# Performance work log

Hardware: AMD Instinct MI355X
Metric: run time of the kernel (lower is better)

## Reference

```python
import jax, jax.numpy as jnp
import numpy as np

P, G, N = 32, 256, 6890  # preds, gallery size, SMPL vertices per person


def _procrustes_v2v(pred, gt):
    """Similarity (Procrustes) align pred->gt, return mean per-vertex L2 error.
    pred, gt: (M, 3) point clouds (M = 2*N, both people jointly aligned)."""
    mu_p = pred.mean(axis=0)
    mu_g = gt.mean(axis=0)
    Xp = pred - mu_p
    Xg = gt - mu_g
    var_p = jnp.sum(Xp * Xp)
    K = Xp.T @ Xg                      # (3,3) cross-covariance
    U, s, Vh = jnp.linalg.svd(K)
    V = Vh.T
    d = jnp.sign(jnp.linalg.det(V @ U.T))  # reflection fix
    D = jnp.stack([jnp.ones_like(d), jnp.ones_like(d), d])
    R = (V * D[None, :]) @ U.T         # rotation, det(R)=+1
    scale = jnp.sum(s * D) / var_p
    aligned = scale * (Xp @ R.T) + mu_g
    return jnp.linalg.norm(aligned - gt, axis=-1).mean()


def setup_inputs() -> dict:
    key = jax.random.key(0)
    k1, k2 = jax.random.split(key)
    pred_vertices = jax.random.normal(k1, (P, 2, N, 3), dtype=jnp.float32)
    target = jax.random.normal(k2, (G, 2, N, 3), dtype=jnp.float32)
    return {"pred_vertices": pred_vertices, "target": target}


def reference(pred_vertices, target):
    # flatten the two-person meshes into a single joint point cloud per sample
    pred = pred_vertices.reshape(pred_vertices.shape[0], -1, 3)  # (P, 2N, 3)
    gt = target.reshape(target.shape[0], -1, 3)                  # (G, 2N, 3)
    # all-pairs procrustes v2v errors: (P, G)
    pair_err = jax.vmap(lambda p: jax.vmap(lambda g: _procrustes_v2v(p, g))(gt))(pred)
    mapping = jnp.argmin(pair_err, axis=1)   # best gt index per prediction
    min_error = jnp.min(pair_err, axis=1)    # its v2v error
    return mapping, min_error
```

## Files before the change

### kernel.cpp

```cpp
#include <hip/hip_runtime.h>
#include <math.h>

#define P_ 32
#define G_ 256
#define NV 6890
#define M_ (2 * NV)
#define QUADS (M_ / 4)
#define NPAIR (P_ * G_)
#define NB_CC 512

typedef float v2f __attribute__((ext_vector_type(2)));
__device__ inline v2f v2(float a, float b) { v2f r; r.x = a; r.y = b; return r; }
__device__ inline v2f vsplat(float a) { v2f r; r.x = a; r.y = a; return r; }
__device__ inline v2f vfma(v2f a, v2f b, v2f c) { return __builtin_elementwise_fma(a, b, c); }

struct WS {
    float mu_p[P_][3];
    float var_p[P_];
    float mu_g[G_][3];
    float At[NPAIR][12];
    float Kmat[NPAIR][9];
    float pair_err[NPAIR];
};

__device__ inline double block_reduce(double v, double* smem) {
#pragma unroll
    for (int off = 32; off > 0; off >>= 1) v += __shfl_down(v, off, 64);
    int wid  = threadIdx.x >> 6;
    int lane = threadIdx.x & 63;
    __syncthreads();
    if (lane == 0) smem[wid] = v;
    __syncthreads();
    double r = 0.0;
    if (threadIdx.x == 0) {
        int nw = blockDim.x >> 6;
        for (int w = 0; w < nw; ++w) r += smem[w];
    }
    return r;
}

__global__ __launch_bounds__(256, 2) void crosscov_p(const float* __restrict__ pred,
                                                     const float* __restrict__ gt,
                                                     WS* __restrict__ ws) {
    int bx = blockIdx.x;
    int t = threadIdx.x;

    if (bx >= NB_CC) {
        int b = bx - NB_CC;
        bool isP = (b < P_);
        const float* base = isP ? pred + (size_t)b * (M_ * 3)
                                : gt + (size_t)(b - P_) * (M_ * 3);
        double sx = 0, sy = 0, sz = 0, sq = 0;
        for (int q = t; q < QUADS; q += 256) {
            const float4* p4 = (const float4*)(base + 12 * (size_t)q);
            float4 a = p4[0], c = p4[1], d = p4[2];
            sx += (double)a.x + (double)a.w + (double)c.z + (double)d.y;
            sy += (double)a.y + (double)c.x + (double)c.w + (double)d.z;
            sz += (double)a.z + (double)c.y + (double)d.x + (double)d.w;
            if (isP) {
                sq += (double)a.x * a.x + (double)a.y * a.y + (double)a.z * a.z +
                      (double)a.w * a.w + (double)c.x * c.x + (double)c.y * c.y +
                      (double)c.z * c.z + (double)c.w * c.w + (double)d.x * d.x +
                      (double)d.y * d.y + (double)d.z * d.z + (double)d.w * d.w;
            }
        }
        __shared__ double smem[4];
        double rx = block_reduce(sx, smem);
        double ry = block_reduce(sy, smem);
        double rz = block_reduce(sz, smem);
        double rq = block_reduce(sq, smem);
        if (t == 0) {
            double mx = rx / M_, my = ry / M_, mz = rz / M_;
            if (isP) {
                ws->mu_p[b][0] = (float)mx;
                ws->mu_p[b][1] = (float)my;
                ws->mu_p[b][2] = (float)mz;
                ws->var_p[b] = (float)(rq - (mx * mx + my * my + mz * mz) * (double)M_);
            } else {
                ws->mu_g[b - P_][0] = (float)mx;
                ws->mu_g[b - P_][1] = (float)my;
                ws->mu_g[b - P_][2] = (float)mz;
            }
        }
        return;
    }

    int gbase = (bx & 63) * 4;
    int pbase = (bx >> 6) * 4;
    const float* pb[4];
    const float* gb[4];
#pragma unroll
    for (int j = 0; j < 4; ++j) {
        pb[j] = pred + (size_t)(pbase + j) * (M_ * 3);
        gb[j] = gt + (size_t)(gbase + j) * (M_ * 3);
    }

    v2f a01[16], a34[16], a67[16], a25[16];
    float a8[16];
#pragma unroll
    for (int i = 0; i < 16; ++i) {
        a01[i] = vsplat(0.f); a34[i] = vsplat(0.f);
        a67[i] = vsplat(0.f); a25[i] = vsplat(0.f);
        a8[i] = 0.f;
    }

    for (int q = t; q < QUADS; q += 256) {
        float4 P[4][3];
#pragma unroll
        for (int j = 0; j < 4; ++j) {
            const float4* p4 = (const float4*)(pb[j] + 12 * (size_t)q);
            P[j][0] = p4[0]; P[j][1] = p4[1]; P[j][2] = p4[2];
        }
#pragma unroll
        for (int gg = 0; gg < 4; ++gg) {
            const float4* g4 = (const float4*)(gb[gg] + 12 * (size_t)q);
            float4 Ga = g4[0], Gc = g4[1], Gd = g4[2];
            v2f gxy0 = v2(Ga.x, Ga.y), gxy1 = v2(Ga.w, Gc.x);
            v2f gxy2 = v2(Gc.z, Gc.w), gxy3 = v2(Gd.y, Gd.z);
            float gz0 = Ga.z, gz1 = Gc.y, gz2 = Gd.x, gz3 = Gd.w;
#pragma unroll
            for (int pp = 0; pp < 4; ++pp) {
                int i = gg * 4 + pp;
                float4 Pa = P[pp][0], Pc = P[pp][1], Pd = P[pp][2];
                a01[i] = vfma(vsplat(Pa.x), gxy0, a01[i]);
                a34[i] = vfma(vsplat(Pa.y), gxy0, a34[i]);
                a67[i] = vfma(vsplat(Pa.z), gxy0, a67[i]);
                a25[i] = vfma(v2(Pa.x, Pa.y), vsplat(gz0), a25[i]);
                a8[i]  = fmaf(Pa.z, gz0, a8[i]);
                a01[i] = vfma(vsplat(Pa.w), gxy1, a01[i]);
                a34[i] = vfma(vsplat(Pc.x), gxy1, a34[i]);
                a67[i] = vfma(vsplat(Pc.y), gxy1, a67[i]);
                a25[i] = vfma(v2(Pa.w, Pc.x), vsplat(gz1), a25[i]);
                a8[i]  = fmaf(Pc.y, gz1, a8[i]);
                a01[i] = vfma(vsplat(Pc.z), gxy2, a01[i]);
                a34[i] = vfma(vsplat(Pc.w), gxy2, a34[i]);
                a67[i] = vfma(vsplat(Pd.x), gxy2, a67[i]);
                a25[i] = vfma(v2(Pc.z, Pc.w), vsplat(gz2), a25[i]);
                a8[i]  = fmaf(Pd.x, gz2, a8[i]);
                a01[i] = vfma(vsplat(Pd.y), gxy3, a01[i]);
                a34[i] = vfma(vsplat(Pd.z), gxy3, a34[i]);
                a67[i] = vfma(vsplat(Pd.w), gxy3, a67[i]);
                a25[i] = vfma(v2(Pd.y, Pd.z), vsplat(gz3), a25[i]);
                a8[i]  = fmaf(Pd.w, gz3, a8[i]);
            }
        }
    }

    float K[16][9];
#pragma unroll
    for (int i = 0; i < 16; ++i) {
        K[i][0] = a01[i].x; K[i][1] = a01[i].y; K[i][2] = a25[i].x;
        K[i][3] = a34[i].x; K[i][4] = a34[i].y; K[i][5] = a25[i].y;
        K[i][6] = a67[i].x; K[i][7] = a67[i].y; K[i][8] = a8[i];
    }

#pragma unroll
    for (int i = 0; i < 16; ++i)
#pragma unroll
        for (int j = 0; j < 9; ++j) {
            float v = K[i][j];
            v += __shfl_xor(v, 1);  v += __shfl_xor(v, 2);
            v += __shfl_xor(v, 4);  v += __shfl_xor(v, 8);
            v += __shfl_xor(v, 16); v += __shfl_xor(v, 32);
            K[i][j] = v;
        }
    __shared__ float part[4][144];
    int lane = t & 63, wave = t >> 6;
    if (lane == 0) {
#pragma unroll
        for (int i = 0; i < 16; ++i)
#pragma unroll
            for (int j = 0; j < 9; ++j) part[wave][i * 9 + j] = K[i][j];
    }
    __syncthreads();
    if (t < 144) {
        float s = part[0][t] + part[1][t] + part[2][t] + part[3][t];
        int idx = t / 9, j = t % 9;
        int gg = idx >> 2, pp = idx & 3;
        ws->Kmat[(gbase + gg) * P_ + (pbase + pp)][j] = s;
    }
}

__global__ __launch_bounds__(256) void pair_svd(WS* ws) {
    int pair = blockIdx.x * blockDim.x + threadIdx.x;
    if (pair >= NPAIR) return;
    int p = pair & 31;
    int g = pair >> 5;

    double K[3][3];
#pragma unroll
    for (int a = 0; a < 3; ++a)
#pragma unroll
        for (int b = 0; b < 3; ++b) K[a][b] = (double)ws->Kmat[pair][3 * a + b];
    {
        double mp[3] = { ws->mu_p[p][0], ws->mu_p[p][1], ws->mu_p[p][2] };
        double mg[3] = { ws->mu_g[g][0], ws->mu_g[g][1], ws->mu_g[g][2] };
#pragma unroll
        for (int a = 0; a < 3; ++a)
#pragma unroll
            for (int b = 0; b < 3; ++b)
                K[a][b] -= (double)M_ * mp[a] * mg[b];
    }

    double S[3][3];
#pragma unroll
    for (int a = 0; a < 3; ++a)
#pragma unroll
        for (int b = 0; b < 3; ++b) {
            double acc = 0.0;
#pragma unroll
            for (int c = 0; c < 3; ++c) acc += K[c][a] * K[c][b];
            S[a][b] = acc;
        }

    double V[3][3] = { {1, 0, 0}, {0, 1, 0}, {0, 0, 1} };
    double tr = S[0][0] + S[1][1] + S[2][2];
    double tol = 1e-30 * tr * tr + 1e-300;
    const int PP[3] = {0, 0, 1};
    const int QQ[3] = {1, 2, 2};
    for (int sweep = 0; sweep < 30; ++sweep) {
        double off = S[0][1] * S[0][1] + S[0][2] * S[0][2] + S[1][2] * S[1][2];
        if (off <= tol) break;
        for (int r3 = 0; r3 < 3; ++r3) {
            int pq = PP[r3], qq = QQ[r3];
            double apq = S[pq][qq];
            if (apq == 0.0) continue;
            double theta = (S[qq][qq] - S[pq][pq]) / (2.0 * apq);
            double tt = copysign(1.0, theta) / (fabs(theta) + sqrt(theta * theta + 1.0));
            double c = 1.0 / sqrt(tt * tt + 1.0);
            double sj = tt * c;
            for (int r = 0; r < 3; ++r) {
                double srp = S[r][pq], srq = S[r][qq];
                S[r][pq] = c * srp - sj * srq;
                S[r][qq] = sj * srp + c * srq;
            }
            for (int cc = 0; cc < 3; ++cc) {
                double spr = S[pq][cc], sqr = S[qq][cc];
                S[pq][cc] = c * spr - sj * sqr;
                S[qq][cc] = sj * spr + c * sqr;
            }
            for (int r = 0; r < 3; ++r) {
                double vrp = V[r][pq], vrq = V[r][qq];
                V[r][pq] = c * vrp - sj * vrq;
                V[r][qq] = sj * vrp + c * vrq;
            }
        }
    }

    double lam[3] = { S[0][0], S[1][1], S[2][2] };
    int idx[3] = { 0, 1, 2 };
    if (lam[idx[0]] < lam[idx[1]]) { int tt = idx[0]; idx[0] = idx[1]; idx[1] = tt; }
    if (lam[idx[0]] < lam[idx[2]]) { int tt = idx[0]; idx[0] = idx[2]; idx[2] = tt; }
    if (lam[idx[1]] < lam[idx[2]]) { int tt = idx[1]; idx[1] = idx[2]; idx[2] = tt; }
    double Vs[3][3];
    double sv[3];
#pragma unroll
    for (int i = 0; i < 3; ++i) {
        double l = lam[idx[i]];
        sv[i] = sqrt(l > 0.0 ? l : 0.0);
        for (int r = 0; r < 3; ++r) Vs[r][i] = V[r][idx[i]];
    }

    double U[3][3];
#pragma unroll
    for (int i = 0; i < 3; ++i) {
        double kx = K[0][0] * Vs[0][i] + K[0][1] * Vs[1][i] + K[0][2] * Vs[2][i];
        double ky = K[1][0] * Vs[0][i] + K[1][1] * Vs[1][i] + K[1][2] * Vs[2][i];
        double kz = K[2][0] * Vs[0][i] + K[2][1] * Vs[1][i] + K[2][2] * Vs[2][i];
        double inv = (sv[i] > 1e-12 * sv[0] && sv[i] > 0.0) ? 1.0 / sv[i] : 0.0;
        U[0][i] = kx * inv; U[1][i] = ky * inv; U[2][i] = kz * inv;
    }
    if (sv[2] <= 1e-12 * sv[0] || sv[0] == 0.0) {
        U[0][2] = U[1][0] * U[2][1] - U[2][0] * U[1][1];
        U[1][2] = U[2][0] * U[0][1] - U[0][0] * U[2][1];
        U[2][2] = U[0][0] * U[1][1] - U[1][0] * U[0][1];
    }

    double detK = K[0][0] * (K[1][1] * K[2][2] - K[1][2] * K[2][1])
                - K[0][1] * (K[1][0] * K[2][2] - K[1][2] * K[2][0])
                + K[0][2] * (K[1][0] * K[2][1] - K[1][1] * K[2][0]);
    double d = (detK >= 0.0) ? 1.0 : -1.0;

    double varp = (double)ws->var_p[p];
    double scale = (sv[0] + sv[1] + d * sv[2]) / varp;

    float A[9];
#pragma unroll
    for (int a = 0; a < 3; ++a)
#pragma unroll
        for (int b = 0; b < 3; ++b) {
            double r = Vs[a][0] * U[b][0] + Vs[a][1] * U[b][1] + d * Vs[a][2] * U[b][2];
            A[3 * a + b] = (float)(scale * r);
        }
    double mp[3] = { ws->mu_p[p][0], ws->mu_p[p][1], ws->mu_p[p][2] };
    double mg[3] = { ws->mu_g[g][0], ws->mu_g[g][1], ws->mu_g[g][2] };
    float tvec[3];
#pragma unroll
    for (int a = 0; a < 3; ++a)
        tvec[a] = (float)(mg[a] - ((double)A[3 * a + 0] * mp[0] + (double)A[3 * a + 1] * mp[1] +
                                   (double)A[3 * a + 2] * mp[2]));

#pragma unroll
    for (int j = 0; j < 9; ++j) ws->At[pair][j] = A[j];
#pragma unroll
    for (int j = 0; j < 3; ++j) ws->At[pair][9 + j] = tvec[j];
}

__global__ __launch_bounds__(256, 3) void pair_error_p(const float* __restrict__ pred,
                                                       const float* __restrict__ gt,
                                                       WS* __restrict__ ws) {
    int bx = blockIdx.x;
    int gbase = (bx & 63) * 4;
    int pbase = (bx >> 6) * 2;
    int t = threadIdx.x;

    v2f a03[8], a14[8], a25v[8], t01[8];
    float a6[8], a7[8], a8v[8], t2[8];
#pragma unroll
    for (int gg = 0; gg < 4; ++gg)
#pragma unroll
        for (int pp = 0; pp < 2; ++pp) {
            int i = gg * 2 + pp;
            const float* At = ws->At[(gbase + gg) * P_ + (pbase + pp)];
            a03[i] = v2(At[0], At[3]);
            a14[i] = v2(At[1], At[4]);
            a25v[i] = v2(At[2], At[5]);
            t01[i] = v2(At[9], At[10]);
            a6[i] = At[6]; a7[i] = At[7]; a8v[i] = At[8]; t2[i] = At[11];
        }

    const float* pb0 = pred + (size_t)pbase * (M_ * 3);
    const float* pb1 = pred + (size_t)(pbase + 1) * (M_ * 3);
    const float* gb[4];
#pragma unroll
    for (int j = 0; j < 4; ++j) gb[j] = gt + (size_t)(gbase + j) * (M_ * 3);

    float acc[8];
#pragma unroll
    for (int i = 0; i < 8; ++i) acc[i] = 0.f;

    for (int q = t; q < QUADS; q += 256) {
        float4 P[2][3];
        {
            const float4* p4 = (const float4*)(pb0 + 12 * (size_t)q);
            P[0][0] = p4[0]; P[0][1] = p4[1]; P[0][2] = p4[2];
            p4 = (const float4*)(pb1 + 12 * (size_t)q);
            P[1][0] = p4[0]; P[1][1] = p4[1]; P[1][2] = p4[2];
        }
#pragma unroll
        for (int gg = 0; gg < 4; ++gg) {
            const float4* g4 = (const float4*)(gb[gg] + 12 * (size_t)q);
            float4 Ga = g4[0], Gc = g4[1], Gd = g4[2];
            v2f gxy[4] = { v2(Ga.x, Ga.y), v2(Ga.w, Gc.x), v2(Gc.z, Gc.w), v2(Gd.y, Gd.z) };
            float gz[4] = { Ga.z, Gc.y, Gd.x, Gd.w };
#pragma unroll
            for (int pp = 0; pp < 2; ++pp) {
                int i = gg * 2 + pp;
                float4 Pa = P[pp][0], Pc = P[pp][1], Pd = P[pp][2];
                float x[4] = { Pa.x, Pa.w, Pc.z, Pd.y };
                float y[4] = { Pa.y, Pc.x, Pc.w, Pd.z };
                float z[4] = { Pa.z, Pc.y, Pd.x, Pd.w };
                float s = 0.f;
#pragma unroll
                for (int k = 0; k < 4; ++k) {
                    v2f dd = vfma(a03[i], vsplat(x[k]),
                             vfma(a14[i], vsplat(y[k]),
                             vfma(a25v[i], vsplat(z[k]), t01[i])));
                    dd = dd - gxy[k];
                    float dz = fmaf(a6[i], x[k], fmaf(a7[i], y[k], fmaf(a8v[i], z[k], t2[i]))) - gz[k];
                    v2f m = dd * dd;
                    s += __builtin_amdgcn_sqrtf(fmaf(dz, dz, m.x + m.y));
                }
                acc[i] += s;
            }
        }
    }

#pragma unroll
    for (int i = 0; i < 8; ++i) {
        float v = acc[i];
        v += __shfl_xor(v, 1);  v += __shfl_xor(v, 2);
        v += __shfl_xor(v, 4);  v += __shfl_xor(v, 8);
        v += __shfl_xor(v, 16); v += __shfl_xor(v, 32);
        acc[i] = v;
    }
    __shared__ float part[4][8];
    int lane = t & 63, wave = t >> 6;
    if (lane == 0) {
#pragma unroll
        for (int i = 0; i < 8; ++i) part[wave][i] = acc[i];
    }
    __syncthreads();
    if (t < 8) {
        float s = part[0][t] + part[1][t] + part[2][t] + part[3][t];
        int gg = t >> 1, pp = t & 1;
        ws->pair_err[(gbase + gg) * P_ + (pbase + pp)] = s / (float)M_;
    }
}

__global__ void argmin_out(const WS* __restrict__ ws, float* __restrict__ out) {
    __shared__ float be[8][32];
    __shared__ int   bg[8][32];
    int t = threadIdx.x;
    int p = t & 31, slice = t >> 5;
    float best = 3.4e38f;
    int bi = G_;
    for (int g = slice; g < G_; g += 8) {
        float e = ws->pair_err[g * P_ + p];
        if (e < best) { best = e; bi = g; }
    }
    be[slice][p] = best;
    bg[slice][p] = bi;
    __syncthreads();
    if (t < P_) {
        float b0 = be[0][t];
        int   i0 = bg[0][t];
        for (int s = 1; s < 8; ++s) {
            float e = be[s][t];
            int   i = bg[s][t];
            if (e < b0 || (e == b0 && i < i0)) { b0 = e; i0 = i; }
        }
        out[t] = (float)i0;
        out[P_ + t] = b0;
    }
}

extern "C" void kernel_launch(void* const* d_in, const int* in_sizes, int n_in,
                              void* d_out, int out_size, void* d_ws, size_t ws_size,
                              hipStream_t stream) {
    const float* pred = (const float*)d_in[0];
    const float* gt   = (const float*)d_in[1];
    float* out = (float*)d_out;
    WS* ws = (WS*)d_ws;

    crosscov_p<<<dim3(NB_CC + P_ + G_), dim3(256), 0, stream>>>(pred, gt, ws);
    pair_svd<<<dim3(NPAIR / 256), dim3(256), 0, stream>>>(ws);
    pair_error_p<<<dim3(16 * 64), dim3(256), 0, stream>>>(pred, gt, ws);
    argmin_out<<<dim3(1), dim3(256), 0, stream>>>(ws, out);
}
```

Measured before the change: 211.8 us.

## Repack point clouds into SoA workspace with fused stats, use in crosscov and error

Adds a repack kernel that transposes each sample's interleaved xyz into a structure-of-arrays copy in the workspace through LDS, and accumulates means and variance with double atomics. The cross-covariance and error kernels then read contiguous X/Y/Z float4 streams instead of strided AoS triples, which removes shuffling of lanes and lets stats run as a separate, better-parallelised pass. pair_svd now uses 64-thread blocks and reads stats directly. The price is an extra full read and write of the inputs (about 30 MB), a memset and an atomic reduction. The old path is kept as a fallback when the workspace is too small.

```diff
diff --git a/kernel.cpp b/kernel.cpp
--- a/kernel.cpp
+++ b/kernel.cpp
@@ -8,6 +8,9 @@
 #define QUADS (M_ / 4)
 #define NPAIR (P_ * G_)
 #define NB_CC 512
+#define SAMPLES (P_ + G_)
+#define NCHUNK 14
+#define SAMPLE_F4 (3 * QUADS)
 
 typedef float v2f __attribute__((ext_vector_type(2)));
 __device__ inline v2f v2(float a, float b) { v2f r; r.x = a; r.y = b; return r; }
@@ -15,6 +18,8 @@
 __device__ inline v2f vfma(v2f a, v2f b, v2f c) { return __builtin_elementwise_fma(a, b, c); }
 
 struct WS {
+    double stat[SAMPLES][4];
+    float soa[SAMPLES * 3 * M_];
     float mu_p[P_][3];
     float var_p[P_];
     float mu_g[G_][3];
@@ -39,60 +44,77 @@
     return r;
 }
 
-__global__ __launch_bounds__(256, 2) void crosscov_p(const float* __restrict__ pred,
-                                                     const float* __restrict__ gt,
-                                                     WS* __restrict__ ws) {
+__global__ __launch_bounds__(256) void repack_stats(const float* __restrict__ pred,
+                                                    const float* __restrict__ gt,
+                                                    WS* __restrict__ ws) {
     int bx = blockIdx.x;
+    int s = bx / NCHUNK;
+    int chunk = bx - s * NCHUNK;
+    bool isP = (s < P_);
+    const float4* src4 = (const float4*)(isP ? pred + (size_t)s * (M_ * 3)
+                                             : gt + (size_t)(s - P_) * (M_ * 3));
+    __shared__ __align__(16) float lds[256 * 12];
     int t = threadIdx.x;
-
-    if (bx >= NB_CC) {
-        int b = bx - NB_CC;
-        bool isP = (b < P_);
-        const float* base = isP ? pred + (size_t)b * (M_ * 3)
-                                : gt + (size_t)(b - P_) * (M_ * 3);
-        double sx = 0, sy = 0, sz = 0, sq = 0;
-        for (int q = t; q < QUADS; q += 256) {
-            const float4* p4 = (const float4*)(base + 12 * (size_t)q);
-            float4 a = p4[0], c = p4[1], d = p4[2];
-            sx += (double)a.x + (double)a.w + (double)c.z + (double)d.y;
-            sy += (double)a.y + (double)c.x + (double)c.w + (double)d.z;
-            sz += (double)a.z + (double)c.y + (double)d.x + (double)d.w;
-            if (isP) {
-                sq += (double)a.x * a.x + (double)a.y * a.y + (double)a.z * a.z +
-                      (double)a.w * a.w + (double)c.x * c.x + (double)c.y * c.y +
-                      (double)c.z * c.z + (double)c.w * c.w + (double)d.x * d.x +
-                      (double)d.y * d.y + (double)d.z * d.z + (double)d.w * d.w;
-            }
-        }
-        __shared__ double smem[4];
-        double rx = block_reduce(sx, smem);
-        double ry = block_reduce(sy, smem);
-        double rz = block_reduce(sz, smem);
-        double rq = block_reduce(sq, smem);
-        if (t == 0) {
-            double mx = rx / M_, my = ry / M_, mz = rz / M_;
-            if (isP) {
-                ws->mu_p[b][0] = (float)mx;
-                ws->mu_p[b][1] = (float)my;
-                ws->mu_p[b][2] = (float)mz;
-                ws->var_p[b] = (float)(rq - (mx * mx + my * my + mz * mz) * (double)M_);
-            } else {
-                ws->mu_g[b - P_][0] = (float)mx;
-                ws->mu_g[b - P_][1] = (float)my;
-                ws->mu_g[b - P_][2] = (float)mz;
-            }
-        }
-        return;
-    }
-
+    int f4base = chunk * (256 * 3);
+#pragma unroll
+    for (int k = 0; k < 3; ++k) {
+        int f4 = f4base + k * 256 + t;
+        if (f4 < SAMPLE_F4) ((float4*)lds)[k * 256 + t] = src4[f4];
+    }
+    __syncthreads();
+    int q = chunk * 256 + t;
+    double sx = 0, sy = 0, sz = 0, sq = 0;
+    if (q < QUADS) {
+        const float* v = lds + 12 * t;
+        float4 X = make_float4(v[0], v[3], v[6], v[9]);
+        float4 Y = make_float4(v[1], v[4], v[7], v[10]);
+        float4 Z = make_float4(v[2], v[5], v[8], v[11]);
+        float4* dst = (float4*)ws->soa;
+        dst[(size_t)(s * 3 + 0) * QUADS + q] = X;
+        dst[(size_t)(s * 3 + 1) * QUADS + q] = Y;
+        dst[(size_t)(s * 3 + 2) * QUADS + q] = Z;
+        sx = (double)X.x + (double)X.y + (double)X.z + (double)X.w;
+        sy = (double)Y.x + (double)Y.y + (double)Y.z + (double)Y.w;
+        sz = (double)Z.x + (double)Z.y + (double)Z.z + (double)Z.w;
+        if (isP) {
+            sq = (double)X.x * X.x + (double)X.y * X.y + (double)X.z * X.z +
+                 (double)X.w * X.w + (double)Y.x * Y.x + (double)Y.y * Y.y +
+                 (double)Y.z * Y.z + (double)Y.w * Y.w + (double)Z.x * Z.x +
+                 (double)Z.y * Z.y + (double)Z.z * Z.z + (double)Z.w * Z.w;
+        }
+    }
+    __shared__ double smem[4];
+    double rx = block_reduce(sx, smem);
+    double ry = block_reduce(sy, smem);
+    double rz = block_reduce(sz, smem);
+    double rq = block_reduce(sq, smem);
+    if (t == 0) {
+        atomicAdd(&ws->stat[s][0], rx);
+        atomicAdd(&ws->stat[s][1], ry);
+        atomicAdd(&ws->stat[s][2], rz);
+        if (isP) atomicAdd(&ws->stat[s][3], rq);
+    }
+}
+
+#define CC_VERT(i, px, py, pz, gxy, gz)                  \
+    a01[i] = vfma(vsplat(px), gxy, a01[i]);              \
+    a34[i] = vfma(vsplat(py), gxy, a34[i]);              \
+    a67[i] = vfma(vsplat(pz), gxy, a67[i]);              \
+    a25[i] = vfma(v2(px, py), vsplat(gz), a25[i]);       \
+    a8[i]  = fmaf(pz, gz, a8[i]);
+
+__global__ __launch_bounds__(256, 2) void crosscov_soa(WS* __restrict__ ws) {
+    int bx = blockIdx.x;
     int gbase = (bx & 63) * 4;
     int pbase = (bx >> 6) * 4;
-    const float* pb[4];
-    const float* gb[4];
+    int t = threadIdx.x;
+    const float4* soa4 = (const float4*)ws->soa;
+    const float4* pb[4];
+    const float4* gb[4];
 #pragma unroll
     for (int j = 0; j < 4; ++j) {
-        pb[j] = pred + (size_t)(pbase + j) * (M_ * 3);
-        gb[j] = gt + (size_t)(gbase + j) * (M_ * 3);
+        pb[j] = soa4 + (size_t)(pbase + j) * SAMPLE_F4;
+        gb[j] = soa4 + (size_t)(P_ + gbase + j) * SAMPLE_F4;
     }
 
     v2f a01[16], a34[16], a67[16], a25[16];
@@ -105,43 +127,27 @@
     }
 
     for (int q = t; q < QUADS; q += 256) {
-        float4 P[4][3];
+        float4 PX[4], PY[4], PZ[4];
 #pragma unroll
         for (int j = 0; j < 4; ++j) {
-            const float4* p4 = (const float4*)(pb[j] + 12 * (size_t)q);
-            P[j][0] = p4[0]; P[j][1] = p4[1]; P[j][2] = p4[2];
+            PX[j] = pb[j][q];
+            PY[j] = pb[j][QUADS + q];
+            PZ[j] = pb[j][2 * QUADS + q];
         }
 #pragma unroll
         for (int gg = 0; gg < 4; ++gg) {
-            const float4* g4 = (const float4*)(gb[gg] + 12 * (size_t)q);
-            float4 Ga = g4[0], Gc = g4[1], Gd = g4[2];
-            v2f gxy0 = v2(Ga.x, Ga.y), gxy1 = v2(Ga.w, Gc.x);
-            v2f gxy2 = v2(Gc.z, Gc.w), gxy3 = v2(Gd.y, Gd.z);
-            float gz0 = Ga.z, gz1 = Gc.y, gz2 = Gd.x, gz3 = Gd.w;
+            float4 GX = gb[gg][q];
+            float4 GY = gb[gg][QUADS + q];
+            float4 GZ = gb[gg][2 * QUADS + q];
+            v2f gxy0 = v2(GX.x, GY.x), gxy1 = v2(GX.y, GY.y);
+            v2f gxy2 = v2(GX.z, GY.z), gxy3 = v2(GX.w, GY.w);
 #pragma unroll
             for (int pp = 0; pp < 4; ++pp) {
                 int i = gg * 4 + pp;
-                float4 Pa = P[pp][0], Pc = P[pp][1], Pd = P[pp][2];
-                a01[i] = vfma(vsplat(Pa.x), gxy0, a01[i]);
-                a34[i] = vfma(vsplat(Pa.y), gxy0, a34[i]);
-                a67[i] = vfma(vsplat(Pa.z), gxy0, a67[i]);
-                a25[i] = vfma(v2(Pa.x, Pa.y), vsplat(gz0), a25[i]);
-                a8[i]  = fmaf(Pa.z, gz0, a8[i]);
-                a01[i] = vfma(vsplat(Pa.w), gxy1, a01[i]);
-                a34[i] = vfma(vsplat(Pc.x), gxy1, a34[i]);
-                a67[i] = vfma(vsplat(Pc.y), gxy1, a67[i]);
-                a25[i] = vfma(v2(Pa.w, Pc.x), vsplat(gz1), a25[i]);
-                a8[i]  = fmaf(Pc.y, gz1, a8[i]);
-                a01[i] = vfma(vsplat(Pc.z), gxy2, a01[i]);
-                a34[i] = vfma(vsplat(Pc.w), gxy2, a34[i]);
-                a67[i] = vfma(vsplat(Pd.x), gxy2, a67[i]);
-                a25[i] = vfma(v2(Pc.z, Pc.w), vsplat(gz2), a25[i]);
-                a8[i]  = fmaf(Pd.x, gz2, a8[i]);
-                a01[i] = vfma(vsplat(Pd.y), gxy3, a01[i]);
-                a34[i] = vfma(vsplat(Pd.z), gxy3, a34[i]);
-                a67[i] = vfma(vsplat(Pd.w), gxy3, a67[i]);
-                a25[i] = vfma(v2(Pd.y, Pd.z), vsplat(gz3), a25[i]);
-                a8[i]  = fmaf(Pd.w, gz3, a8[i]);
+                CC_VERT(i, PX[pp].x, PY[pp].x, PZ[pp].x, gxy0, GZ.x)
+                CC_VERT(i, PX[pp].y, PY[pp].y, PZ[pp].y, gxy1, GZ.y)
+                CC_VERT(i, PX[pp].z, PY[pp].z, PZ[pp].z, gxy2, GZ.z)
+                CC_VERT(i, PX[pp].w, PY[pp].w, PZ[pp].w, gxy3, GZ.w)
             }
         }
     }
@@ -153,7 +159,6 @@
         K[i][3] = a34[i].x; K[i][4] = a34[i].y; K[i][5] = a25[i].y;
         K[i][6] = a67[i].x; K[i][7] = a67[i].y; K[i][8] = a8[i];
     }
-
 #pragma unroll
     for (int i = 0; i < 16; ++i)
 #pragma unroll
@@ -181,26 +186,34 @@
     }
 }
 
-__global__ __launch_bounds__(256) void pair_svd(WS* ws) {
+__global__ void pair_svd(WS* __restrict__ ws, int use_stat) {
     int pair = blockIdx.x * blockDim.x + threadIdx.x;
     if (pair >= NPAIR) return;
     int p = pair & 31;
     int g = pair >> 5;
 
+    double mp[3], mg[3], varp;
+    if (use_stat) {
+        const double invM = 1.0 / (double)M_;
+        mp[0] = ws->stat[p][0] * invM;
+        mp[1] = ws->stat[p][1] * invM;
+        mp[2] = ws->stat[p][2] * invM;
+        mg[0] = ws->stat[P_ + g][0] * invM;
+        mg[1] = ws->stat[P_ + g][1] * invM;
+        mg[2] = ws->stat[P_ + g][2] * invM;
+        varp = ws->stat[p][3] - (mp[0] * mp[0] + mp[1] * mp[1] + mp[2] * mp[2]) * (double)M_;
+    } else {
+        mp[0] = ws->mu_p[p][0]; mp[1] = ws->mu_p[p][1]; mp[2] = ws->mu_p[p][2];
+        mg[0] = ws->mu_g[g][0]; mg[1] = ws->mu_g[g][1]; mg[2] = ws->mu_g[g][2];
+        varp = (double)ws->var_p[p];
+    }
+
     double K[3][3];
 #pragma unroll
     for (int a = 0; a < 3; ++a)
 #pragma unroll
-        for (int b = 0; b < 3; ++b) K[a][b] = (double)ws->Kmat[pair][3 * a + b];
-    {
-        double mp[3] = { ws->mu_p[p][0], ws->mu_p[p][1], ws->mu_p[p][2] };
-        double mg[3] = { ws->mu_g[g][0], ws->mu_g[g][1], ws->mu_g[g][2] };
-#pragma unroll
-        for (int a = 0; a < 3; ++a)
-#pragma unroll
-            for (int b = 0; b < 3; ++b)
-                K[a][b] -= (double)M_ * mp[a] * mg[b];
-    }
+        for (int b = 0; b < 3; ++b)
+            K[a][b] = (double)ws->Kmat[pair][3 * a + b] - (double)M_ * mp[a] * mg[b];
 
     double S[3][3];
 #pragma unroll
@@ -280,8 +293,6 @@
                 - K[0][1] * (K[1][0] * K[2][2] - K[1][2] * K[2][0])
                 + K[0][2] * (K[1][0] * K[2][1] - K[1][1] * K[2][0]);
     double d = (detK >= 0.0) ? 1.0 : -1.0;
-
-    double varp = (double)ws->var_p[p];
     double scale = (sv[0] + sv[1] + d * sv[2]) / varp;
 
     float A[9];
@@ -292,8 +303,6 @@
             double r = Vs[a][0] * U[b][0] + Vs[a][1] * U[b][1] + d * Vs[a][2] * U[b][2];
             A[3 * a + b] = (float)(scale * r);
         }
-    double mp[3] = { ws->mu_p[p][0], ws->mu_p[p][1], ws->mu_p[p][2] };
-    double mg[3] = { ws->mu_g[g][0], ws->mu_g[g][1], ws->mu_g[g][2] };
     float tvec[3];
 #pragma unroll
     for (int a = 0; a < 3; ++a)
@@ -306,9 +315,7 @@
     for (int j = 0; j < 3; ++j) ws->At[pair][9 + j] = tvec[j];
 }
 
-__global__ __launch_bounds__(256, 3) void pair_error_p(const float* __restrict__ pred,
-                                                       const float* __restrict__ gt,
-                                                       WS* __restrict__ ws) {
+__global__ __launch_bounds__(256, 3) void pair_error_soa(WS* __restrict__ ws) {
     int bx = blockIdx.x;
     int gbase = (bx & 63) * 4;
     int pbase = (bx >> 6) * 2;
@@ -329,37 +336,39 @@
             a6[i] = At[6]; a7[i] = At[7]; a8v[i] = At[8]; t2[i] = At[11];
         }
 
-    const float* pb0 = pred + (size_t)pbase * (M_ * 3);
-    const float* pb1 = pred + (size_t)(pbase + 1) * (M_ * 3);
-    const float* gb[4];
-#pragma unroll
-    for (int j = 0; j < 4; ++j) gb[j] = gt + (size_t)(gbase + j) * (M_ * 3);
+    const float4* soa4 = (const float4*)ws->soa;
+    const float4* pb[2];
+    const float4* gb[4];
+#pragma unroll
+    for (int j = 0; j < 2; ++j) pb[j] = soa4 + (size_t)(pbase + j) * SAMPLE_F4;
+#pragma unroll
+    for (int j = 0; j < 4; ++j) gb[j] = soa4 + (size_t)(P_ + gbase + j) * SAMPLE_F4;
 
     float acc[8];
 #pragma unroll
     for (int i = 0; i < 8; ++i) acc[i] = 0.f;
 
     for (int q = t; q < QUADS; q += 256) {
-        float4 P[2][3];
-        {
-            const float4* p4 = (const float4*)(pb0 + 12 * (size_t)q);
-            P[0][0] = p4[0]; P[0][1] = p4[1]; P[0][2] = p4[2];
-            p4 = (const float4*)(pb1 + 12 * (size_t)q);
-            P[1][0] = p4[0]; P[1][1] = p4[1]; P[1][2] = p4[2];
+        float4 PX[2], PY[2], PZ[2];
+#pragma unroll
+        for (int j = 0; j < 2; ++j) {
+            PX[j] = pb[j][q];
+            PY[j] = pb[j][QUADS + q];
+            PZ[j] = pb[j][2 * QUADS + q];
         }
 #pragma unroll
         for (int gg = 0; gg < 4; ++gg) {
-            const float4* g4 = (const float4*)(gb[gg] + 12 * (size_t)q);
-            float4 Ga = g4[0], Gc = g4[1], Gd = g4[2];
-            v2f gxy[4] = { v2(Ga.x, Ga.y), v2(Ga.w, Gc.x), v2(Gc.z, Gc.w), v2(Gd.y, Gd.z) };
-            float gz[4] = { Ga.z, Gc.y, Gd.x, Gd.w };
+            float4 GX = gb[gg][q];
+            float4 GY = gb[gg][QUADS + q];
+            float4 GZ = gb[gg][2 * QUADS + q];
+            v2f gxy[4] = { v2(GX.x, GY.x), v2(GX.y, GY.y), v2(GX.z, GY.z), v2(GX.w, GY.w) };
+            float gz[4] = { GZ.x, GZ.y, GZ.z, GZ.w };
 #pragma unroll
             for (int pp = 0; pp < 2; ++pp) {
                 int i = gg * 2 + pp;
-                float4 Pa = P[pp][0], Pc = P[pp][1], Pd = P[pp][2];
-                float x[4] = { Pa.x, Pa.w, Pc.z, Pd.y };
-                float y[4] = { Pa.y, Pc.x, Pc.w, Pd.z };
-                float z[4] = { Pa.z, Pc.y, Pd.x, Pd.w };
+                float x[4] = { PX[pp].x, PX[pp].y, PX[pp].z, PX[pp].w };
+                float y[4] = { PY[pp].x, PY[pp].y, PY[pp].z, PY[pp].w };
+                float z[4] = { PZ[pp].x, PZ[pp].y, PZ[pp].z, PZ[pp].w };
                 float s = 0.f;
 #pragma unroll
                 for (int k = 0; k < 4; ++k) {
@@ -425,6 +434,223 @@
     }
 }
 
+__global__ __launch_bounds__(256, 2) void crosscov_p(const float* __restrict__ pred,
+                                                     const float* __restrict__ gt,
+                                                     WS* __restrict__ ws) {
+    int bx = blockIdx.x;
+    int t = threadIdx.x;
+
+    if (bx >= NB_CC) {
+        int b = bx - NB_CC;
+        bool isP = (b < P_);
+        const float* base = isP ? pred + (size_t)b * (M_ * 3)
+                                : gt + (size_t)(b - P_) * (M_ * 3);
+        double sx = 0, sy = 0, sz = 0, sq = 0;
+        for (int q = t; q < QUADS; q += 256) {
+            const float4* p4 = (const float4*)(base + 12 * (size_t)q);
+            float4 a = p4[0], c = p4[1], d = p4[2];
+            sx += (double)a.x + (double)a.w + (double)c.z + (double)d.y;
+            sy += (double)a.y + (double)c.x + (double)c.w + (double)d.z;
+            sz += (double)a.z + (double)c.y + (double)d.x + (double)d.w;
+            if (isP) {
+                sq += (double)a.x * a.x + (double)a.y * a.y + (double)a.z * a.z +
+                      (double)a.w * a.w + (double)c.x * c.x + (double)c.y * c.y +
+                      (double)c.z * c.z + (double)c.w * c.w + (double)d.x * d.x +
+                      (double)d.y * d.y + (double)d.z * d.z + (double)d.w * d.w;
+            }
+        }
+        __shared__ double smem[4];
+        double rx = block_reduce(sx, smem);
+        double ry = block_reduce(sy, smem);
+        double rz = block_reduce(sz, smem);
+        double rq = block_reduce(sq, smem);
+        if (t == 0) {
+            double mx = rx / M_, my = ry / M_, mz = rz / M_;
+            if (isP) {
+                ws->mu_p[b][0] = (float)mx;
+                ws->mu_p[b][1] = (float)my;
+                ws->mu_p[b][2] = (float)mz;
+                ws->var_p[b] = (float)(rq - (mx * mx + my * my + mz * mz) * (double)M_);
+            } else {
+                ws->mu_g[b - P_][0] = (float)mx;
+                ws->mu_g[b - P_][1] = (float)my;
+                ws->mu_g[b - P_][2] = (float)mz;
+            }
+        }
+        return;
+    }
+
+    int gbase = (bx & 63) * 4;
+    int pbase = (bx >> 6) * 4;
+    const float* pb[4];
+    const float* gb[4];
+#pragma unroll
+    for (int j = 0; j < 4; ++j) {
+        pb[j] = pred + (size_t)(pbase + j) * (M_ * 3);
+        gb[j] = gt + (size_t)(gbase + j) * (M_ * 3);
+    }
+
+    v2f a01[16], a34[16], a67[16], a25[16];
+    float a8[16];
+#pragma unroll
+    for (int i = 0; i < 16; ++i) {
+        a01[i] = vsplat(0.f); a34[i] = vsplat(0.f);
+        a67[i] = vsplat(0.f); a25[i] = vsplat(0.f);
+        a8[i] = 0.f;
+    }
+
+    for (int q = t; q < QUADS; q += 256) {
+        float4 P[4][3];
+#pragma unroll
+        for (int j = 0; j < 4; ++j) {
+            const float4* p4 = (const float4*)(pb[j] + 12 * (size_t)q);
+            P[j][0] = p4[0]; P[j][1] = p4[1]; P[j][2] = p4[2];
+        }
+#pragma unroll
+        for (int gg = 0; gg < 4; ++gg) {
+            const float4* g4 = (const float4*)(gb[gg] + 12 * (size_t)q);
+            float4 Ga = g4[0], Gc = g4[1], Gd = g4[2];
+            v2f gxy0 = v2(Ga.x, Ga.y), gxy1 = v2(Ga.w, Gc.x);
+            v2f gxy2 = v2(Gc.z, Gc.w), gxy3 = v2(Gd.y, Gd.z);
+            float gz0 = Ga.z, gz1 = Gc.y, gz2 = Gd.x, gz3 = Gd.w;
+#pragma unroll
+            for (int pp = 0; pp < 4; ++pp) {
+                int i = gg * 4 + pp;
+                float4 Pa = P[pp][0], Pc = P[pp][1], Pd = P[pp][2];
+                CC_VERT(i, Pa.x, Pa.y, Pa.z, gxy0, gz0)
+                CC_VERT(i, Pa.w, Pc.x, Pc.y, gxy1, gz1)
+                CC_VERT(i, Pc.z, Pc.w, Pd.x, gxy2, gz2)
+                CC_VERT(i, Pd.y, Pd.z, Pd.w, gxy3, gz3)
+            }
+        }
+    }
+
+    float K[16][9];
+#pragma unroll
+    for (int i = 0; i < 16; ++i) {
+        K[i][0] = a01[i].x; K[i][1] = a01[i].y; K[i][2] = a25[i].x;
+        K[i][3] = a34[i].x; K[i][4] = a34[i].y; K[i][5] = a25[i].y;
+        K[i][6] = a67[i].x; K[i][7] = a67[i].y; K[i][8] = a8[i];
+    }
+#pragma unroll
+    for (int i = 0; i < 16; ++i)
+#pragma unroll
+        for (int j = 0; j < 9; ++j) {
+            float v = K[i][j];
+            v += __shfl_xor(v, 1);  v += __shfl_xor(v, 2);
+            v += __shfl_xor(v, 4);  v += __shfl_xor(v, 8);
+            v += __shfl_xor(v, 16); v += __shfl_xor(v, 32);
+            K[i][j] = v;
+        }
+    __shared__ float part[4][144];
+    int lane = t & 63, wave = t >> 6;
+    if (lane == 0) {
+#pragma unroll
+        for (int i = 0; i < 16; ++i)
+#pragma unroll
+            for (int j = 0; j < 9; ++j) part[wave][i * 9 + j] = K[i][j];
+    }
+    __syncthreads();
+    if (t < 144) {
+        float s = part[0][t] + part[1][t] + part[2][t] + part[3][t];
+        int idx = t / 9, j = t % 9;
+        int gg = idx >> 2, pp = idx & 3;
+        ws->Kmat[(gbase + gg) * P_ + (pbase + pp)][j] = s;
+    }
+}
+
+__global__ __launch_bounds__(256, 3) void pair_error_p(const float* __restrict__ pred,
+                                                       const float* __restrict__ gt,
+                                                       WS* __restrict__ ws) {
+    int bx = blockIdx.x;
+    int gbase = (bx & 63) * 4;
+    int pbase = (bx >> 6) * 2;
+    int t = threadIdx.x;
+
+    v2f a03[8], a14[8], a25v[8], t01[8];
+    float a6[8], a7[8], a8v[8], t2[8];
+#pragma unroll
+    for (int gg = 0; gg < 4; ++gg)
+#pragma unroll
+        for (int pp = 0; pp < 2; ++pp) {
+            int i = gg * 2 + pp;
+            const float* At = ws->At[(gbase + gg) * P_ + (pbase + pp)];
+            a03[i] = v2(At[0], At[3]);
+            a14[i] = v2(At[1], At[4]);
+            a25v[i] = v2(At[2], At[5]);
+            t01[i] = v2(At[9], At[10]);
+            a6[i] = At[6]; a7[i] = At[7]; a8v[i] = At[8]; t2[i] = At[11];
+        }
+
+    const float* pb0 = pred + (size_t)pbase * (M_ * 3);
+    const float* pb1 = pred + (size_t)(pbase + 1) * (M_ * 3);
+    const float* gb[4];
+#pragma unroll
+    for (int j = 0; j < 4; ++j) gb[j] = gt + (size_t)(gbase + j) * (M_ * 3);
+
+    float acc[8];
+#pragma unroll
+    for (int i = 0; i < 8; ++i) acc[i] = 0.f;
+
+    for (int q = t; q < QUADS; q += 256) {
+        float4 P[2][3];
+        {
+            const float4* p4 = (const float4*)(pb0 + 12 * (size_t)q);
+            P[0][0] = p4[0]; P[0][1] = p4[1]; P[0][2] = p4[2];
+            p4 = (const float4*)(pb1 + 12 * (size_t)q);
+            P[1][0] = p4[0]; P[1][1] = p4[1]; P[1][2] = p4[2];
+        }
+#pragma unroll
+        for (int gg = 0; gg < 4; ++gg) {
+            const float4* g4 = (const float4*)(gb[gg] + 12 * (size_t)q);
+            float4 Ga = g4[0], Gc = g4[1], Gd = g4[2];
+            v2f gxy[4] = { v2(Ga.x, Ga.y), v2(Ga.w, Gc.x), v2(Gc.z, Gc.w), v2(Gd.y, Gd.z) };
+            float gz[4] = { Ga.z, Gc.y, Gd.x, Gd.w };
+#pragma unroll
+            for (int pp = 0; pp < 2; ++pp) {
+                int i = gg * 2 + pp;
+                float4 Pa = P[pp][0], Pc = P[pp][1], Pd = P[pp][2];
+                float x[4] = { Pa.x, Pa.w, Pc.z, Pd.y };
+                float y[4] = { Pa.y, Pc.x, Pc.w, Pd.z };
+                float z[4] = { Pa.z, Pc.y, Pd.x, Pd.w };
+                float s = 0.f;
+#pragma unroll
+                for (int k = 0; k < 4; ++k) {
+                    v2f dd = vfma(a03[i], vsplat(x[k]),
+                             vfma(a14[i], vsplat(y[k]),
+                             vfma(a25v[i], vsplat(z[k]), t01[i])));
+                    dd = dd - gxy[k];
+                    float dz = fmaf(a6[i], x[k], fmaf(a7[i], y[k], fmaf(a8v[i], z[k], t2[i]))) - gz[k];
+                    v2f m = dd * dd;
+                    s += __builtin_amdgcn_sqrtf(fmaf(dz, dz, m.x + m.y));
+                }
+                acc[i] += s;
+            }
+        }
+    }
+
+#pragma unroll
+    for (int i = 0; i < 8; ++i) {
+        float v = acc[i];
+        v += __shfl_xor(v, 1);  v += __shfl_xor(v, 2);
+        v += __shfl_xor(v, 4);  v += __shfl_xor(v, 8);
+        v += __shfl_xor(v, 16); v += __shfl_xor(v, 32);
+        acc[i] = v;
+    }
+    __shared__ float part[4][8];
+    int lane = t & 63, wave = t >> 6;
+    if (lane == 0) {
+#pragma unroll
+        for (int i = 0; i < 8; ++i) part[wave][i] = acc[i];
+    }
+    __syncthreads();
+    if (t < 8) {
+        float s = part[0][t] + part[1][t] + part[2][t] + part[3][t];
+        int gg = t >> 1, pp = t & 1;
+        ws->pair_err[(gbase + gg) * P_ + (pbase + pp)] = s / (float)M_;
+    }
+}
+
 extern "C" void kernel_launch(void* const* d_in, const int* in_sizes, int n_in,
                               void* d_out, int out_size, void* d_ws, size_t ws_size,
                               hipStream_t stream) {
@@ -433,8 +659,17 @@
     float* out = (float*)d_out;
     WS* ws = (WS*)d_ws;
 
-    crosscov_p<<<dim3(NB_CC + P_ + G_), dim3(256), 0, stream>>>(pred, gt, ws);
-    pair_svd<<<dim3(NPAIR / 256), dim3(256), 0, stream>>>(ws);
-    pair_error_p<<<dim3(16 * 64), dim3(256), 0, stream>>>(pred, gt, ws);
-    argmin_out<<<dim3(1), dim3(256), 0, stream>>>(ws, out);
-}
+    if (ws_size >= sizeof(WS)) {
+        hipMemsetAsync(d_ws, 0, sizeof(double) * SAMPLES * 4, stream);
+        repack_stats<<<dim3(SAMPLES * NCHUNK), dim3(256), 0, stream>>>(pred, gt, ws);
+        crosscov_soa<<<dim3(NB_CC), dim3(256), 0, stream>>>(ws);
+        pair_svd<<<dim3(NPAIR / 64), dim3(64), 0, stream>>>(ws, 1);
+        pair_error_soa<<<dim3(16 * 64), dim3(256), 0, stream>>>(ws);
+        argmin_out<<<dim3(1), dim3(256), 0, stream>>>(ws, out);
+    } else {
+        crosscov_p<<<dim3(NB_CC + P_ + G_), dim3(256), 0, stream>>>(pred, gt, ws);
+        pair_svd<<<dim3(NPAIR / 64), dim3(64), 0, stream>>>(ws, 0);
+        pair_error_p<<<dim3(16 * 64), dim3(256), 0, stream>>>(pred, gt, ws);
+        argmin_out<<<dim3(1), dim3(256), 0, stream>>>(ws, out);
+    }
+}
```

Measured after the change: 282.0 us. 33.1% more time.

## Restructure cross-covariance kernel with LDS-staged gallery chunks and wave-per-prediction tiling

Applied to the files above, without the earlier changes.

The cross-covariance kernel now uses 512-thread blocks. Each block stages 4 gallery clouds in shared memory, split into x/y/z planes and processed in chunks of 128 quads. Each of the 8 waves handles one prediction and writes its 4 K matrices directly, with no cross-wave reduction. Fewer registers go to accumulators (4 pairs per thread instead of 16) in exchange for LDS traffic and two barriers per chunk. The SVD kernel also moves to 64-thread blocks for more blocks per GPU and hoists its mean loads.

```diff
diff --git a/kernel.cpp b/kernel.cpp
--- a/kernel.cpp
+++ b/kernel.cpp
@@ -7,7 +7,9 @@
 #define M_ (2 * NV)
 #define QUADS (M_ / 4)
 #define NPAIR (P_ * G_)
-#define NB_CC 512
+#define NB_WS 256
+#define CHUNK_Q 128
+#define NCHUNKS ((QUADS + CHUNK_Q - 1) / CHUNK_Q)
 
 typedef float v2f __attribute__((ext_vector_type(2)));
 __device__ inline v2f v2(float a, float b) { v2f r; r.x = a; r.y = b; return r; }
@@ -39,19 +41,19 @@
     return r;
 }
 
-__global__ __launch_bounds__(256, 2) void crosscov_p(const float* __restrict__ pred,
-                                                     const float* __restrict__ gt,
-                                                     WS* __restrict__ ws) {
+__global__ __launch_bounds__(512) void crosscov_ws(const float* __restrict__ pred,
+                                                   const float* __restrict__ gt,
+                                                   WS* __restrict__ ws) {
     int bx = blockIdx.x;
     int t = threadIdx.x;
 
-    if (bx >= NB_CC) {
-        int b = bx - NB_CC;
+    if (bx >= NB_WS) {
+        int b = bx - NB_WS;
         bool isP = (b < P_);
         const float* base = isP ? pred + (size_t)b * (M_ * 3)
                                 : gt + (size_t)(b - P_) * (M_ * 3);
         double sx = 0, sy = 0, sz = 0, sq = 0;
-        for (int q = t; q < QUADS; q += 256) {
+        for (int q = t; q < QUADS; q += 512) {
             const float4* p4 = (const float4*)(base + 12 * (size_t)q);
             float4 a = p4[0], c = p4[1], d = p4[2];
             sx += (double)a.x + (double)a.w + (double)c.z + (double)d.y;
@@ -64,7 +66,7 @@
                       (double)d.y * d.y + (double)d.z * d.z + (double)d.w * d.w;
             }
         }
-        __shared__ double smem[4];
+        __shared__ double smem[8];
         double rx = block_reduce(sx, smem);
         double ry = block_reduce(sy, smem);
         double rz = block_reduce(sz, smem);
@@ -86,76 +88,85 @@
     }
 
     int gbase = (bx & 63) * 4;
-    int pbase = (bx >> 6) * 4;
-    const float* pb[4];
-    const float* gb[4];
-#pragma unroll
-    for (int j = 0; j < 4; ++j) {
-        pb[j] = pred + (size_t)(pbase + j) * (M_ * 3);
-        gb[j] = gt + (size_t)(gbase + j) * (M_ * 3);
-    }
-
-    v2f a01[16], a34[16], a67[16], a25[16];
-    float a8[16];
-#pragma unroll
-    for (int i = 0; i < 16; ++i) {
+    int pbase = (bx >> 6) * 8;
+    int wave = t >> 6;
+    int lane = t & 63;
+    int p = pbase + wave;
+
+    const float* pb = pred + (size_t)p * (M_ * 3);
+    int ss = t >> 7;
+    int si = t & 127;
+    const float4* gsrc = (const float4*)(gt + (size_t)(gbase + ss) * (M_ * 3));
+
+    __shared__ __align__(16) float glds[3][4][CHUNK_Q * 4];
+
+    v2f a01[4], a34[4], a67[4], a25[4];
+    float a8[4];
+#pragma unroll
+    for (int i = 0; i < 4; ++i) {
         a01[i] = vsplat(0.f); a34[i] = vsplat(0.f);
         a67[i] = vsplat(0.f); a25[i] = vsplat(0.f);
         a8[i] = 0.f;
     }
 
-    for (int q = t; q < QUADS; q += 256) {
-        float4 P[4][3];
-#pragma unroll
-        for (int j = 0; j < 4; ++j) {
-            const float4* p4 = (const float4*)(pb[j] + 12 * (size_t)q);
-            P[j][0] = p4[0]; P[j][1] = p4[1]; P[j][2] = p4[2];
-        }
-#pragma unroll
-        for (int gg = 0; gg < 4; ++gg) {
-            const float4* g4 = (const float4*)(gb[gg] + 12 * (size_t)q);
-            float4 Ga = g4[0], Gc = g4[1], Gd = g4[2];
-            v2f gxy0 = v2(Ga.x, Ga.y), gxy1 = v2(Ga.w, Gc.x);
-            v2f gxy2 = v2(Gc.z, Gc.w), gxy3 = v2(Gd.y, Gd.z);
-            float gz0 = Ga.z, gz1 = Gc.y, gz2 = Gd.x, gz3 = Gd.w;
-#pragma unroll
-            for (int pp = 0; pp < 4; ++pp) {
-                int i = gg * 4 + pp;
-                float4 Pa = P[pp][0], Pc = P[pp][1], Pd = P[pp][2];
-                a01[i] = vfma(vsplat(Pa.x), gxy0, a01[i]);
-                a34[i] = vfma(vsplat(Pa.y), gxy0, a34[i]);
-                a67[i] = vfma(vsplat(Pa.z), gxy0, a67[i]);
-                a25[i] = vfma(v2(Pa.x, Pa.y), vsplat(gz0), a25[i]);
-                a8[i]  = fmaf(Pa.z, gz0, a8[i]);
-                a01[i] = vfma(vsplat(Pa.w), gxy1, a01[i]);
-                a34[i] = vfma(vsplat(Pc.x), gxy1, a34[i]);
-                a67[i] = vfma(vsplat(Pc.y), gxy1, a67[i]);
-                a25[i] = vfma(v2(Pa.w, Pc.x), vsplat(gz1), a25[i]);
-                a8[i]  = fmaf(Pc.y, gz1, a8[i]);
-                a01[i] = vfma(vsplat(Pc.z), gxy2, a01[i]);
-                a34[i] = vfma(vsplat(Pc.w), gxy2, a34[i]);
-                a67[i] = vfma(vsplat(Pd.x), gxy2, a67[i]);
-                a25[i] = vfma(v2(Pc.z, Pc.w), vsplat(gz2), a25[i]);
-                a8[i]  = fmaf(Pd.x, gz2, a8[i]);
-                a01[i] = vfma(vsplat(Pd.y), gxy3, a01[i]);
-                a34[i] = vfma(vsplat(Pd.z), gxy3, a34[i]);
-                a67[i] = vfma(vsplat(Pd.w), gxy3, a67[i]);
-                a25[i] = vfma(v2(Pd.y, Pd.z), vsplat(gz3), a25[i]);
-                a8[i]  = fmaf(Pd.w, gz3, a8[i]);
-            }
-        }
-    }
-
-    float K[16][9];
-#pragma unroll
-    for (int i = 0; i < 16; ++i) {
+    for (int c = 0; c < NCHUNKS; ++c) {
+        int qb = c * CHUNK_Q;
+        int nq = QUADS - qb; if (nq > CHUNK_Q) nq = CHUNK_Q;
+        __syncthreads();
+#pragma unroll
+        for (int r = 0; r < 3; ++r) {
+            int fi = si + r * 128;
+            if (fi < 3 * nq) {
+                float4 v = gsrc[(size_t)qb * 3 + fi];
+                float vv[4] = { v.x, v.y, v.z, v.w };
+#pragma unroll
+                for (int j = 0; j < 4; ++j) {
+                    int f = 4 * fi + j;
+                    glds[f % 3][ss][f / 3] = vv[j];
+                }
+            }
+        }
+        __syncthreads();
+#pragma unroll
+        for (int sub = 0; sub < 2; ++sub) {
+            int qq = lane + sub * 64;
+            if (qq < nq) {
+                const float4* p4 = (const float4*)(pb + 12 * (size_t)(qb + qq));
+                float4 Pa = p4[0], Pc = p4[1], Pd = p4[2];
+                float x[4] = { Pa.x, Pa.w, Pc.z, Pd.y };
+                float y[4] = { Pa.y, Pc.x, Pc.w, Pd.z };
+                float z[4] = { Pa.z, Pc.y, Pd.x, Pd.w };
+#pragma unroll
+                for (int gg = 0; gg < 4; ++gg) {
+                    float4 GX = *(const float4*)&glds[0][gg][4 * qq];
+                    float4 GY = *(const float4*)&glds[1][gg][4 * qq];
+                    float4 GZ = *(const float4*)&glds[2][gg][4 * qq];
+                    float gxv[4] = { GX.x, GX.y, GX.z, GX.w };
+                    float gyv[4] = { GY.x, GY.y, GY.z, GY.w };
+                    float gzv[4] = { GZ.x, GZ.y, GZ.z, GZ.w };
+#pragma unroll
+                    for (int k = 0; k < 4; ++k) {
+                        v2f gxy = v2(gxv[k], gyv[k]);
+                        a01[gg] = vfma(vsplat(x[k]), gxy, a01[gg]);
+                        a34[gg] = vfma(vsplat(y[k]), gxy, a34[gg]);
+                        a67[gg] = vfma(vsplat(z[k]), gxy, a67[gg]);
+                        a25[gg] = vfma(v2(x[k], y[k]), vsplat(gzv[k]), a25[gg]);
+                        a8[gg]  = fmaf(z[k], gzv[k], a8[gg]);
+                    }
+                }
+            }
+        }
+    }
+
+    float K[4][9];
+#pragma unroll
+    for (int i = 0; i < 4; ++i) {
         K[i][0] = a01[i].x; K[i][1] = a01[i].y; K[i][2] = a25[i].x;
         K[i][3] = a34[i].x; K[i][4] = a34[i].y; K[i][5] = a25[i].y;
         K[i][6] = a67[i].x; K[i][7] = a67[i].y; K[i][8] = a8[i];
     }
-
-#pragma unroll
-    for (int i = 0; i < 16; ++i)
+#pragma unroll
+    for (int i = 0; i < 4; ++i)
 #pragma unroll
         for (int j = 0; j < 9; ++j) {
             float v = K[i][j];
@@ -164,43 +175,31 @@
             v += __shfl_xor(v, 16); v += __shfl_xor(v, 32);
             K[i][j] = v;
         }
-    __shared__ float part[4][144];
-    int lane = t & 63, wave = t >> 6;
     if (lane == 0) {
 #pragma unroll
-        for (int i = 0; i < 16; ++i)
-#pragma unroll
-            for (int j = 0; j < 9; ++j) part[wave][i * 9 + j] = K[i][j];
-    }
-    __syncthreads();
-    if (t < 144) {
-        float s = part[0][t] + part[1][t] + part[2][t] + part[3][t];
-        int idx = t / 9, j = t % 9;
-        int gg = idx >> 2, pp = idx & 3;
-        ws->Kmat[(gbase + gg) * P_ + (pbase + pp)][j] = s;
-    }
-}
-
-__global__ __launch_bounds__(256) void pair_svd(WS* ws) {
+        for (int gg = 0; gg < 4; ++gg)
+#pragma unroll
+            for (int j = 0; j < 9; ++j)
+                ws->Kmat[(gbase + gg) * P_ + p][j] = K[gg][j];
+    }
+}
+
+__global__ void pair_svd(WS* __restrict__ ws) {
     int pair = blockIdx.x * blockDim.x + threadIdx.x;
     if (pair >= NPAIR) return;
     int p = pair & 31;
     int g = pair >> 5;
 
+    double mp[3] = { ws->mu_p[p][0], ws->mu_p[p][1], ws->mu_p[p][2] };
+    double mg[3] = { ws->mu_g[g][0], ws->mu_g[g][1], ws->mu_g[g][2] };
+    double varp = (double)ws->var_p[p];
+
     double K[3][3];
 #pragma unroll
     for (int a = 0; a < 3; ++a)
 #pragma unroll
-        for (int b = 0; b < 3; ++b) K[a][b] = (double)ws->Kmat[pair][3 * a + b];
-    {
-        double mp[3] = { ws->mu_p[p][0], ws->mu_p[p][1], ws->mu_p[p][2] };
-        double mg[3] = { ws->mu_g[g][0], ws->mu_g[g][1], ws->mu_g[g][2] };
-#pragma unroll
-        for (int a = 0; a < 3; ++a)
-#pragma unroll
-            for (int b = 0; b < 3; ++b)
-                K[a][b] -= (double)M_ * mp[a] * mg[b];
-    }
+        for (int b = 0; b < 3; ++b)
+            K[a][b] = (double)ws->Kmat[pair][3 * a + b] - (double)M_ * mp[a] * mg[b];
 
     double S[3][3];
 #pragma unroll
@@ -280,8 +279,6 @@
                 - K[0][1] * (K[1][0] * K[2][2] - K[1][2] * K[2][0])
                 + K[0][2] * (K[1][0] * K[2][1] - K[1][1] * K[2][0]);
     double d = (detK >= 0.0) ? 1.0 : -1.0;
-
-    double varp = (double)ws->var_p[p];
     double scale = (sv[0] + sv[1] + d * sv[2]) / varp;
 
     float A[9];
@@ -292,8 +289,6 @@
             double r = Vs[a][0] * U[b][0] + Vs[a][1] * U[b][1] + d * Vs[a][2] * U[b][2];
             A[3 * a + b] = (float)(scale * r);
         }
-    double mp[3] = { ws->mu_p[p][0], ws->mu_p[p][1], ws->mu_p[p][2] };
-    double mg[3] = { ws->mu_g[g][0], ws->mu_g[g][1], ws->mu_g[g][2] };
     float tvec[3];
 #pragma unroll
     for (int a = 0; a < 3; ++a)
@@ -433,8 +428,8 @@
     float* out = (float*)d_out;
     WS* ws = (WS*)d_ws;
 
-    crosscov_p<<<dim3(NB_CC + P_ + G_), dim3(256), 0, stream>>>(pred, gt, ws);
-    pair_svd<<<dim3(NPAIR / 256), dim3(256), 0, stream>>>(ws);
+    crosscov_ws<<<dim3(NB_WS + P_ + G_), dim3(512), 0, stream>>>(pred, gt, ws);
+    pair_svd<<<dim3(NPAIR / 64), dim3(64), 0, stream>>>(ws);
     pair_error_p<<<dim3(16 * 64), dim3(256), 0, stream>>>(pred, gt, ws);
     argmin_out<<<dim3(1), dim3(256), 0, stream>>>(ws, out);
 }
```

After: 223.5 us. 5.5% more time.
